# Optimization experiments

Measured on AMD Instinct MI355X. Metric: run time of the kernel, lower is better.

The kernel has to match this reference:

```python
import jax, jax.numpy as jnp
import numpy as np

K_STEPS = 2  # number of staged propagation levels encoded in edge_mask


def _propagate(h, src, dst, mask, num_nodes):
    """KPropagate: K staged scatter-add steps over the edge list.

    Step k sums messages along edges with edge_mask == k; later steps
    propagate the freshly aggregated values (rule-node fan-out).
    """
    out = jnp.zeros_like(h)
    cur = h
    for k in range(K_STEPS):
        msg = jnp.where((mask == k)[:, None], cur[src], jnp.zeros((), h.dtype))  # [E, F]
        out = out + jax.ops.segment_sum(msg, dst, num_segments=num_nodes)
        cur = out
    return out


def setup_inputs() -> dict:
    key = jax.random.key(0)
    ks = jax.random.split(key, 8)
    V, R = 50000, 10000
    N = V + R
    E = 160000
    F_IN, F_OUT = 512, 128
    x = jax.random.normal(ks[0], (N, F_IN), dtype=jnp.float32)
    edge_index = jax.random.randint(ks[1], (2, E), 0, N, dtype=jnp.int64)
    edge_mask = jax.random.randint(ks[2], (E,), 0, K_STEPS, dtype=jnp.int64)
    # lin1: in_features -> in_features; lin2: in_features -> out_features
    s1 = 1.0 / np.sqrt(F_IN)
    W1 = jax.random.uniform(ks[3], (F_IN, F_IN), jnp.float32, -s1, s1)
    b1 = jax.random.uniform(ks[4], (F_IN,), jnp.float32, -s1, s1)
    W2 = jax.random.uniform(ks[5], (F_IN, F_OUT), jnp.float32, -s1, s1)
    b2 = jax.random.uniform(ks[6], (F_OUT,), jnp.float32, -s1, s1)
    return {"x": x, "edge_index": edge_index, "edge_mask": edge_mask,
            "vertex_cnt": V, "rule_cnt": R,
            "W1": W1, "b1": b1, "W2": W2, "b2": b2}


def reference(x, edge_index, edge_mask, vertex_cnt, rule_cnt, W1, b1, W2, b2):
    N = x.shape[0]  # == vertex_cnt + rule_cnt
    src, dst = edge_index[0], edge_index[1]
    h = x @ W1 + b1                                   # lin1
    h = jax.nn.relu(_propagate(h, src, dst, edge_mask, N))  # P1 -> relu
    h = h @ W2 + b2                                   # lin2
    h = _propagate(h, src, dst, edge_mask, N)         # P2
    # NOTE: original code computes log_softmax into `out` but returns x (=h).
    return h
```

## Files before the change

### kernel.cpp

```cpp
#include <hip/hip_runtime.h>

typedef __bf16 bf16x8 __attribute__((ext_vector_type(8)));
typedef float  floatx4 __attribute__((ext_vector_type(4)));
typedef unsigned short ushortx8 __attribute__((ext_vector_type(8)));
typedef unsigned short ushortx4 __attribute__((ext_vector_type(4)));
typedef unsigned short ushortx2 __attribute__((ext_vector_type(2)));

__device__ __forceinline__ float bf2f(unsigned short u) {
    return __uint_as_float(((unsigned)u) << 16);
}
__device__ __forceinline__ unsigned short f2bf(float f) {
    unsigned u = __float_as_uint(f);
    return (unsigned short)((u + 0x7FFFu + ((u >> 16) & 1u)) >> 16);
}

__device__ __forceinline__ void gload_lds16(const unsigned short* g, unsigned short* l) {
    __builtin_amdgcn_global_load_lds(
        (const __attribute__((address_space(1))) void*)g,
        (__attribute__((address_space(3))) void*)l, 16, 0, 0);
}

#define NKT 8

__device__ __forceinline__ size_t staged_chunk(int r, int c ) {
    int tile = r >> 7, rt = r & 127;
    int g = rt >> 4, mrow = rt & 15;
    int kti = c >> 3, c7 = c & 7;
    int s = c7 >> 2, q = c7 & 3;
    return (((size_t)tile * NKT + kti) << 13) + ((size_t)(s * 8 + g) << 9)
         + ((size_t)((q << 4) | mrow) << 3);
}

__global__ __launch_bounds__(256) void prep_kernel(
    const float* __restrict__ x,  unsigned short* __restrict__ xb,  int nchunk, int bc,
    const float* __restrict__ W1, unsigned short* __restrict__ W1t, int bw1,
    const float* __restrict__ W2, unsigned short* __restrict__ W2t, int bw2,
    int* __restrict__ head, int nhead, int FIN, int FOUT)
{
    const int bid = blockIdx.x, tid = threadIdx.x;
    if (bid < bc) {
        int i = bid * 256 + tid;
        if (i < nchunk) {
            int r = i >> 6, c = i & 63;
            float4 v0 = ((const float4*)x)[i * 2];
            float4 v1 = ((const float4*)x)[i * 2 + 1];
            ushortx8 o;
            o[0] = f2bf(v0.x); o[1] = f2bf(v0.y); o[2] = f2bf(v0.z); o[3] = f2bf(v0.w);
            o[4] = f2bf(v1.x); o[5] = f2bf(v1.y); o[6] = f2bf(v1.z); o[7] = f2bf(v1.w);
            *(ushortx8*)(xb + staged_chunk(r, c)) = o;
        }
    } else if (bid < bc + bw1) {
        int idx = (bid - bc) * 256 + tid;
        if (idx < FIN * FIN) {
            int k = idx / FIN, n = idx - k * FIN;
            W1t[staged_chunk(n, k >> 3) + (k & 7)] = f2bf(W1[idx]);
        }
    } else if (bid < bc + bw1 + bw2) {
        int idx = (bid - bc - bw1) * 256 + tid;
        if (idx < FIN * FOUT) {
            int k = idx / FOUT, n = idx - k * FOUT;
            W2t[staged_chunk(n, k >> 3) + (k & 7)] = f2bf(W2[idx]);
        }
    } else {
        int i = (bid - bc - bw1 - bw2) * 256 + tid;
        if (i < nhead) head[i] = -1;
    }
}

__global__ void build_list_kernel(const int* __restrict__ ei, const int* __restrict__ em,
                                  int E, int Nn,
                                  int* __restrict__ head, int* __restrict__ nxt) {
    int e = blockIdx.x * blockDim.x + threadIdx.x;
    if (e >= E) return;
    int d = ei[E + e];
    int m = em[e];
    nxt[e] = atomicExch(&head[m * Nn + d], e);
}

#define BM 128
#define BN 128

__global__ __launch_bounds__(256, 4) void gemm_bt_bias(
    const unsigned short* __restrict__ A,
    const unsigned short* __restrict__ Bt,
    const float* __restrict__ bias,
    unsigned short* __restrict__ C,
    int M, int N, int K)
{
    __shared__ unsigned short Sh[16384];
    unsigned short (*As)[512] = (unsigned short(*)[512])Sh;
    unsigned short (*Bs)[512] = (unsigned short(*)[512])(Sh + 8192);

    const int tid  = threadIdx.x;
    const int lane = tid & 63;
    const int wave = tid >> 6;

    int bx, by;
    if (gridDim.x == 4) {
        int id = blockIdx.y * 4 + blockIdx.x;
        int full = (gridDim.y & ~7) * 4;
        if (id < full) {
            bx = (id >> 3) & 3;
            by = (id >> 5) * 8 + (id & 7);
        } else {
            int t = id - full;
            by = (gridDim.y & ~7) + (t >> 2);
            bx = t & 3;
        }
    } else {
        bx = blockIdx.x; by = blockIdx.y;
    }
    const int bM = by * BM;
    const int bN = bx * BN;
    const int wm = (wave >> 1) * 64;
    const int wn = (wave & 1) * 64;
    const int q    = lane >> 4;
    const int mrow = lane & 15;

    const unsigned short* as_ = A  + (((size_t)by * NKT) << 13) + (wave << 11) + (lane << 3);
    const unsigned short* bs_ = Bt + (((size_t)bx * NKT) << 13) + (wave << 11) + (lane << 3);

    floatx4 acc[4][4];
#pragma unroll
    for (int i = 0; i < 4; i++)
#pragma unroll
        for (int j = 0; j < 4; j++) acc[i][j] = (floatx4)(0.0f);

    for (int t = 0; t < NKT; ++t) {
#pragma unroll
        for (int c = 0; c < 4; c++) {
            gload_lds16(as_ + (c << 9), Sh + (wave << 11) + (c << 9));
            gload_lds16(bs_ + (c << 9), Sh + 8192 + (wave << 11) + (c << 9));
        }
        __syncthreads();

#pragma unroll
        for (int s = 0; s < 2; s++) {
            bf16x8 af[4], bfv[4];
#pragma unroll
            for (int mi = 0; mi < 4; mi++)
                af[mi] = *(const bf16x8*)&As[s * 8 + (wave >> 1) * 4 + mi][lane * 8];
#pragma unroll
            for (int ni = 0; ni < 4; ni++)
                bfv[ni] = *(const bf16x8*)&Bs[s * 8 + (wave & 1) * 4 + ni][lane * 8];
#pragma unroll
            for (int mi = 0; mi < 4; mi++)
#pragma unroll
                for (int ni = 0; ni < 4; ni++)
                    acc[mi][ni] = __builtin_amdgcn_mfma_f32_16x16x32_bf16(
                        af[mi], bfv[ni], acc[mi][ni], 0, 0, 0);
        }
        __syncthreads();
        as_ += 8192; bs_ += 8192;
    }

    unsigned short* lbuf = Sh + wave * 2048;
    float bv[4];
#pragma unroll
    for (int ni = 0; ni < 4; ni++) bv[ni] = bias[bN + wn + ni * 16 + mrow];

#pragma unroll
    for (int p = 0; p < 2; p++) {
#pragma unroll
        for (int mh = 0; mh < 2; mh++) {
            int mi = 2 * p + mh;
#pragma unroll
            for (int ni = 0; ni < 4; ni++)
#pragma unroll
                for (int r = 0; r < 4; r++)
                    lbuf[(mh * 16 + q * 4 + r) * 64 + ni * 16 + mrow] =
                        f2bf(acc[mi][ni][r] + bv[ni]);
        }
#pragma unroll
        for (int i = 0; i < 4; i++) {
            int prow = i * 8 + (lane >> 3);
            int pcol = (lane & 7) * 8;
            int grow = bM + wm + p * 32 + prow;
            if (grow < M)
                *(ushortx8*)(C + (size_t)grow * N + bN + wn + pcol) =
                    *(const ushortx8*)&lbuf[prow * 64 + pcol];
        }
    }
}

template <int VEC> struct VecT;
template <> struct VecT<8> { typedef ushortx8 type; };
template <> struct VecT<2> { typedef ushortx2 type; };

template <int VEC, bool ADD_SELF, bool RELU, bool OUT_F32, bool OUT_STAGED = false>
__global__ __launch_bounds__(256, 8) void prop_step_kernel(
    const unsigned short* __restrict__ cur,
    void* __restrict__ outp,
    const int* __restrict__ head,
    const int* __restrict__ nxt,
    const int* __restrict__ esrc,
    int Nn)
{
    typedef typename VecT<VEC>::type VT;
    const int w = blockIdx.x * 4 + (threadIdx.x >> 6);
    if (w >= Nn) return;
    const int lane = threadIdx.x & 63;
    const int F = VEC * 64;
    const size_t off = (size_t)w * F + lane * VEC;

    float acc[VEC];
    if (ADD_SELF) {
        VT v = *(const VT*)(cur + off);
#pragma unroll
        for (int i = 0; i < VEC; i++) acc[i] = bf2f(v[i]);
    } else {
#pragma unroll
        for (int i = 0; i < VEC; i++) acc[i] = 0.0f;
    }

    for (int e = head[w]; e >= 0; e = nxt[e]) {
        int s = esrc[e];
        VT v = *(const VT*)(cur + (size_t)s * F + lane * VEC);
#pragma unroll
        for (int i = 0; i < VEC; i++) acc[i] += bf2f(v[i]);
    }

#pragma unroll
    for (int i = 0; i < VEC; i++)
        if (RELU && acc[i] < 0.0f) acc[i] = 0.0f;

    if (OUT_F32) {
        float* out = (float*)outp;
        float2 o2;
#pragma unroll
        for (int i = 0; i < VEC; i += 2) {
            o2.x = acc[i]; o2.y = acc[i + 1];
            *(float2*)(out + off + i) = o2;
        }
    } else {
        VT o;
#pragma unroll
        for (int i = 0; i < VEC; i++) o[i] = f2bf(acc[i]);
        if (OUT_STAGED && VEC == 8) {
            *(VT*)((unsigned short*)outp + staged_chunk(w, lane)) = o;
        } else {
            *(VT*)((unsigned short*)outp + off) = o;
        }
    }
}

extern "C" void kernel_launch(void* const* d_in, const int* in_sizes, int n_in,
                              void* d_out, int out_size, void* d_ws, size_t ws_size,
                              hipStream_t stream)
{
    const float* x  = (const float*)d_in[0];
    const int*   ei = (const int*)d_in[1];
    const int*   em = (const int*)d_in[2];
    const float* W1 = (const float*)d_in[5];
    const float* b1 = (const float*)d_in[6];
    const float* W2 = (const float*)d_in[7];
    const float* b2 = (const float*)d_in[8];

    const int FIN = 512, FOUT = 128;
    const int Nn = in_sizes[0] / FIN;
    const int E  = in_sizes[2];
    const int Mpad = ((Nn + 127) >> 7) << 7;

    char* ws = (char*)d_ws;
    size_t off = 0;
    auto alloc = [&](size_t bytes) -> char* {
        char* p = ws + off;
        off += (bytes + 255) & ~(size_t)255;
        return p;
    };
    unsigned short* W1t = (unsigned short*)alloc((size_t)FIN * FIN * 2);
    unsigned short* W2t = (unsigned short*)alloc((size_t)FIN * FOUT * 2);
    unsigned short* xb  = (unsigned short*)alloc((size_t)Mpad * FIN * 2);
    unsigned short* h1  = (unsigned short*)alloc((size_t)Mpad * FIN * 2);
    unsigned short* h2  = (unsigned short*)alloc((size_t)Nn * FOUT * 2);
    unsigned short* A2  = (unsigned short*)alloc((size_t)Nn * FOUT * 2);
    int* head = (int*)alloc((size_t)2 * Nn * 4);
    int* nxt  = (int*)alloc((size_t)E * 4);
    unsigned short* A1 = xb;
    (void)ws_size; (void)n_in; (void)out_size;

    {
        int nchunk = Nn * (FIN / 8);
        int bc  = (nchunk + 255) / 256;
        int bw1 = (FIN * FIN + 255) / 256;
        int bw2 = (FIN * FOUT + 255) / 256;
        int bh  = (2 * Nn + 255) / 256;
        prep_kernel<<<bc + bw1 + bw2 + bh, 256, 0, stream>>>(
            x, xb, nchunk, bc, W1, W1t, bw1, W2, W2t, bw2, head, 2 * Nn, FIN, FOUT);
    }

    build_list_kernel<<<(E + 255) / 256, 256, 0, stream>>>(ei, em, E, Nn, head, nxt);

    {
        dim3 grid(FIN / BN, Mpad / BM);
        gemm_bt_bias<<<grid, 256, 0, stream>>>(xb, W1t, b1, h1, Nn, FIN, FIN);
    }

    {
        int grid = (Nn + 3) / 4;
        prop_step_kernel<8, false, false, false, false><<<grid, 256, 0, stream>>>(
            h1, A1, head, nxt, ei, Nn);
        prop_step_kernel<8, true,  true,  false, true ><<<grid, 256, 0, stream>>>(
            A1, h1, head + Nn, nxt, ei, Nn);
    }

    {
        dim3 grid(FOUT / BN, Mpad / BM);
        gemm_bt_bias<<<grid, 256, 0, stream>>>(h1, W2t, b2, h2, Nn, FOUT, FIN);
    }

    {
        int grid = (Nn + 3) / 4;
        prop_step_kernel<2, false, false, false><<<grid, 256, 0, stream>>>(
            h2, A2, head, nxt, ei, Nn);
        prop_step_kernel<2, true,  false, true ><<<grid, 256, 0, stream>>>(
            A2, d_out, head + Nn, nxt, ei, Nn);
    }
}
```

Measured before the change: 385.4 us.

## Fuse two propagation steps into one cooperative kernel with grid sync

Replaces each pair of propagation-step launches with a single cooperative kernel. The kernel processes nodes in a grid-stride loop, does a grid-wide sync, then runs the second step. The goal is to drop one kernel launch and its inter-kernel gap per propagation. The cost is a fixed grid of 2048 blocks, which must all be co-resident for the cooperative launch to work, and the overhead of the grid barrier.

```diff
diff --git a/kernel.cpp b/kernel.cpp
--- a/kernel.cpp
+++ b/kernel.cpp
@@ -1,4 +1,7 @@
 #include <hip/hip_runtime.h>
+#include <hip/hip_cooperative_groups.h>
+
+namespace cg = cooperative_groups;
 
 typedef __bf16 bf16x8 __attribute__((ext_vector_type(8)));
 typedef float  floatx4 __attribute__((ext_vector_type(4)));
@@ -187,9 +190,10 @@
 template <> struct VecT<8> { typedef ushortx8 type; };
 template <> struct VecT<2> { typedef ushortx2 type; };
 
-template <int VEC, bool ADD_SELF, bool RELU, bool OUT_F32, bool OUT_STAGED = false>
-__global__ __launch_bounds__(256, 8) void prop_step_kernel(
+template <int VEC, bool RELU, bool OUT_F32, bool OUT_STAGED>
+__global__ __launch_bounds__(256, 8) void prop_fused_kernel(
     const unsigned short* __restrict__ cur,
+    unsigned short* __restrict__ mid,
     void* __restrict__ outp,
     const int* __restrict__ head,
     const int* __restrict__ nxt,
@@ -197,49 +201,62 @@
     int Nn)
 {
     typedef typename VecT<VEC>::type VT;
-    const int w = blockIdx.x * 4 + (threadIdx.x >> 6);
-    if (w >= Nn) return;
     const int lane = threadIdx.x & 63;
     const int F = VEC * 64;
-    const size_t off = (size_t)w * F + lane * VEC;
-
-    float acc[VEC];
-    if (ADD_SELF) {
-        VT v = *(const VT*)(cur + off);
-#pragma unroll
-        for (int i = 0; i < VEC; i++) acc[i] = bf2f(v[i]);
-    } else {
+    const int wstart = blockIdx.x * 4 + (threadIdx.x >> 6);
+    const int wstep  = gridDim.x * 4;
+
+    for (int w = wstart; w < Nn; w += wstep) {
+        float acc[VEC];
 #pragma unroll
         for (int i = 0; i < VEC; i++) acc[i] = 0.0f;
-    }
-
-    for (int e = head[w]; e >= 0; e = nxt[e]) {
-        int s = esrc[e];
-        VT v = *(const VT*)(cur + (size_t)s * F + lane * VEC);
-#pragma unroll
-        for (int i = 0; i < VEC; i++) acc[i] += bf2f(v[i]);
-    }
-
-#pragma unroll
-    for (int i = 0; i < VEC; i++)
-        if (RELU && acc[i] < 0.0f) acc[i] = 0.0f;
-
-    if (OUT_F32) {
-        float* out = (float*)outp;
-        float2 o2;
-#pragma unroll
-        for (int i = 0; i < VEC; i += 2) {
-            o2.x = acc[i]; o2.y = acc[i + 1];
-            *(float2*)(out + off + i) = o2;
-        }
-    } else {
+        for (int e = head[w]; e >= 0; e = nxt[e]) {
+            int s = esrc[e];
+            VT v = *(const VT*)(cur + (size_t)s * F + lane * VEC);
+#pragma unroll
+            for (int i = 0; i < VEC; i++) acc[i] += bf2f(v[i]);
+        }
         VT o;
 #pragma unroll
         for (int i = 0; i < VEC; i++) o[i] = f2bf(acc[i]);
-        if (OUT_STAGED && VEC == 8) {
-            *(VT*)((unsigned short*)outp + staged_chunk(w, lane)) = o;
+        *(VT*)(mid + (size_t)w * F + lane * VEC) = o;
+    }
+
+    cg::this_grid().sync();
+
+    for (int w = wstart; w < Nn; w += wstep) {
+        const size_t off = (size_t)w * F + lane * VEC;
+        VT sv = *(const VT*)(mid + off);
+        float acc[VEC];
+#pragma unroll
+        for (int i = 0; i < VEC; i++) acc[i] = bf2f(sv[i]);
+        for (int e = head[Nn + w]; e >= 0; e = nxt[e]) {
+            int s = esrc[e];
+            VT v = *(const VT*)(mid + (size_t)s * F + lane * VEC);
+#pragma unroll
+            for (int i = 0; i < VEC; i++) acc[i] += bf2f(v[i]);
+        }
+#pragma unroll
+        for (int i = 0; i < VEC; i++)
+            if (RELU && acc[i] < 0.0f) acc[i] = 0.0f;
+
+        if (OUT_F32) {
+            float* out = (float*)outp;
+            float2 o2;
+#pragma unroll
+            for (int i = 0; i < VEC; i += 2) {
+                o2.x = acc[i]; o2.y = acc[i + 1];
+                *(float2*)(out + off + i) = o2;
+            }
         } else {
-            *(VT*)((unsigned short*)outp + off) = o;
+            VT o;
+#pragma unroll
+            for (int i = 0; i < VEC; i++) o[i] = f2bf(acc[i]);
+            if (OUT_STAGED && VEC == 8) {
+                *(VT*)((unsigned short*)outp + staged_chunk(w, lane)) = o;
+            } else {
+                *(VT*)((unsigned short*)outp + off) = o;
+            }
         }
     }
 }
@@ -297,11 +314,18 @@
     }
 
     {
-        int grid = (Nn + 3) / 4;
-        prop_step_kernel<8, false, false, false, false><<<grid, 256, 0, stream>>>(
-            h1, A1, head, nxt, ei, Nn);
-        prop_step_kernel<8, true,  true,  false, true ><<<grid, 256, 0, stream>>>(
-            A1, h1, head + Nn, nxt, ei, Nn);
+        const unsigned short* cur = h1;
+        unsigned short* mid = A1;
+        void* outp = (void*)h1;
+        const int* hd = head;
+        const int* nx = nxt;
+        const int* es = ei;
+        int nn = Nn;
+        void* args[] = {(void*)&cur, (void*)&mid, (void*)&outp,
+                        (void*)&hd, (void*)&nx, (void*)&es, (void*)&nn};
+        hipLaunchCooperativeKernel(
+            (const void*)&prop_fused_kernel<8, true, false, true>,
+            dim3(2048), dim3(256), args, 0, stream);
     }
 
     {
@@ -310,10 +334,17 @@
     }
 
     {
-        int grid = (Nn + 3) / 4;
-        prop_step_kernel<2, false, false, false><<<grid, 256, 0, stream>>>(
-            h2, A2, head, nxt, ei, Nn);
-        prop_step_kernel<2, true,  false, true ><<<grid, 256, 0, stream>>>(
-            A2, d_out, head + Nn, nxt, ei, Nn);
-    }
-}
+        const unsigned short* cur = h2;
+        unsigned short* mid = A2;
+        void* outp = d_out;
+        const int* hd = head;
+        const int* nx = nxt;
+        const int* es = ei;
+        int nn = Nn;
+        void* args[] = {(void*)&cur, (void*)&mid, (void*)&outp,
+                        (void*)&hd, (void*)&nx, (void*)&es, (void*)&nn};
+        hipLaunchCooperativeKernel(
+            (const void*)&prop_fused_kernel<2, false, true, false>,
+            dim3(2048), dim3(256), args, 0, stream);
+    }
+}
```

Measured after the change: 885.2 us. 130% more time.
